# Kernel tuning notes

Hardware: AMD Instinct MI355X
Metric: run time of the kernel (lower is better)

The kernel has to match this reference:

```python
import jax, jax.numpy as jnp
import numpy as np

IN, OUT, RANK = 512, 1024, 8
STEPS = 8  # fixed-step RK4 integration of the geodesic ODE over t in [0, 1]


def setup_inputs() -> dict:
    key = jax.random.key(0)
    ks = jax.random.split(key, 8)
    scale = 0.05
    x = jax.random.normal(ks[0], (8, 4096, IN), jnp.float32)
    # orthogonal init of U_0 [OUT, IN] (orthonormal columns, tall matrix)
    U0 = jnp.linalg.qr(jax.random.normal(ks[1], (OUT, IN), jnp.float32))[0]
    Wa = scale * jax.random.normal(ks[2], (IN, RANK), jnp.float32)
    La = scale * jax.random.normal(ks[3], (IN, RANK), jnp.float32)
    Ra = scale * jax.random.normal(ks[4], (IN, RANK), jnp.float32)
    Wb = scale * jax.random.normal(ks[5], (IN, RANK), jnp.float32)
    Lb = scale * jax.random.normal(ks[6], (OUT - IN, RANK), jnp.float32)
    Rb = scale * jax.random.normal(ks[7], (IN, RANK), jnp.float32)
    return {"x": x, "U0": U0, "Wa": Wa, "La": La, "Ra": Ra,
            "Wb": Wb, "Lb": Lb, "Rb": Rb}


def _geodesic_solve(U0, A, G):
    # Integrate dU/dt = U @ A + G, U(0) = U0, with RK4 over unit time.
    dt = 1.0 / STEPS
    f = lambda U: U @ A + G
    def step(U, _):
        k1 = f(U)
        k2 = f(U + 0.5 * dt * k1)
        k3 = f(U + 0.5 * dt * k2)
        k4 = f(U + dt * k3)
        return U + (dt / 6.0) * (k1 + 2.0 * k2 + 2.0 * k3 + k4), None
    U, _ = jax.lax.scan(step, U0, None, length=STEPS)
    return U


def reference(x, U0, Wa, La, Ra, Wb, Lb, Rb):
    # z: pooled context [B, IN]
    z = x.mean(axis=1)
    # low-rank controller -> skew-symmetric Lie-algebra drift A [IN, IN]
    a = z @ Wa                                      # [B, R]
    A = jnp.einsum('br,ir,jr->bij', a, La, Ra)      # [B, IN, IN]
    A_avg = (A - jnp.swapaxes(A, 1, 2)).mean(axis=0)  # skew, batch-averaged
    # low-rank forcing B [B, OUT-IN, IN], batch-averaged
    b = z @ Wb                                      # [B, R]
    B_avg = jnp.einsum('br,or,jr->boj', b, Lb, Rb).mean(axis=0)
    # pad top with zeros -> G [OUT, IN]
    G = jnp.concatenate([jnp.zeros((IN, IN), x.dtype), B_avg], axis=0)
    # geodesic/Lie ODE solve for the dynamic weight W [OUT, IN]
    W = _geodesic_solve(U0, A_avg, G)
    # final dense projection
    return x @ W.T
```

## Files before the change

### kernel.cpp

```cpp
#include <hip/hip_runtime.h>
#include <hip/hip_bf16.h>
#include <type_traits>
#include <cstdint>

#define IN_DIM   512
#define OUT_DIM  1024
#define MROWS    32768

typedef float f32x4 __attribute__((ext_vector_type(4)));
typedef short s8vec __attribute__((ext_vector_type(8)));
typedef __bf16 b8vec __attribute__((ext_vector_type(8)));

template <typename V, typename = void>
struct mfma_ok : std::false_type {};
template <typename V>
struct mfma_ok<V, std::void_t<decltype(__builtin_amdgcn_mfma_f32_16x16x32_bf16(
    std::declval<V>(), std::declval<V>(), std::declval<f32x4>(), 0, 0, 0))>>
    : std::true_type {};
using frag_t = std::conditional_t<mfma_ok<s8vec>::value, s8vec, b8vec>;

__device__ __forceinline__ void async_copy16(void* lds, const void* g) {
    __builtin_amdgcn_global_load_lds(
        (const __attribute__((address_space(1))) void*)(uintptr_t)g,
        (__attribute__((address_space(3))) void*)(uint32_t)(uintptr_t)lds,
        16, 0, 0);
}

__device__ __forceinline__ unsigned short f2bf(float f) {
    unsigned int u = __float_as_uint(f);
    unsigned int r = (u + 0x7fffu + ((u >> 16) & 1u)) >> 16;
    return (unsigned short)r;
}

__global__ void __launch_bounds__(256) geo_k1(const float* __restrict__ x,
                                              unsigned short* __restrict__ xh,
                                              const float* __restrict__ Wa,
                                              const float* __restrict__ Wb,
                                              float* __restrict__ part) {
    const int tid  = threadIdx.x;
    const int c4   = (tid & 127) * 4;
    const int half = tid >> 7;
    const int r0   = blockIdx.x * 32 + half * 16;
    float4 s = {0.f, 0.f, 0.f, 0.f};
    for (int i = 0; i < 16; ++i) {
        const size_t base = (size_t)(r0 + i) * IN_DIM + c4;
        float4 v = *(const float4*)(x + base);
        s.x += v.x; s.y += v.y; s.z += v.z; s.w += v.w;
        ushort4 h;
        h.x = f2bf(v.x); h.y = f2bf(v.y); h.z = f2bf(v.z); h.w = f2bf(v.w);
        *(ushort4*)(xh + base) = h;
    }
    const float* wa = Wa + (size_t)c4 * 8;
    const float* wb = Wb + (size_t)c4 * 8;
    float av[8], bv[8];
#pragma unroll
    for (int r = 0; r < 8; ++r) {
        av[r] = s.x * wa[r] + s.y * wa[8 + r] + s.z * wa[16 + r] + s.w * wa[24 + r];
        bv[r] = s.x * wb[r] + s.y * wb[8 + r] + s.z * wb[16 + r] + s.w * wb[24 + r];
    }
#pragma unroll
    for (int off = 32; off; off >>= 1) {
#pragma unroll
        for (int r = 0; r < 8; ++r) {
            av[r] += __shfl_xor(av[r], off, 64);
            bv[r] += __shfl_xor(bv[r], off, 64);
        }
    }
    __shared__ float wred[4][16];
    const int lane = tid & 63, wave = tid >> 6;
    if (lane == 0) {
#pragma unroll
        for (int r = 0; r < 8; ++r) { wred[wave][r] = av[r]; wred[wave][8 + r] = bv[r]; }
    }
    __syncthreads();
    if (tid < 16)
        part[(size_t)blockIdx.x * 16 + tid] =
            wred[0][tid] + wred[1][tid] + wred[2][tid] + wred[3][tid];
}

__device__ __forceinline__ void mm16(float (*D)[16], float (*A)[16], float (*B)[16]) {
    const int tid = threadIdx.x;
    const int i = tid >> 4, j = tid & 15;
    float s = 0.f;
#pragma unroll
    for (int k = 0; k < 16; ++k) s += A[i][k] * B[k][j];
    __syncthreads();
    D[i][j] = s;
    __syncthreads();
}

__global__ void __launch_bounds__(256) geo_k2(const float* __restrict__ part,
                                              const float* __restrict__ La,
                                              const float* __restrict__ Ra,
                                              const float* __restrict__ Lb,
                                              const float* __restrict__ Rb,
                                              float* __restrict__ Vws,
                                              float* __restrict__ Lbp,
                                              float* __restrict__ VPws,
                                              float* __restrict__ RRws) {
    __shared__ float sV[IN_DIM][16];
    __shared__ float sRb[IN_DIM][8];
    __shared__ float red2[16][16];
    __shared__ float gs[16];
    __shared__ float G16[16][16], Jm[16][16];
    __shared__ float C2m[16][16], C3m[16][16], C4m[16][16];
    __shared__ float Cp[16][16], Cq[16][16];
    __shared__ float Pi[16][16], Xi[16][16], T1[16][16], T2[16][16], Ct[16][16];
    __shared__ float Zm[8][16], Em[8][16];
    const int tid = threadIdx.x;
    const int i = tid >> 4, j = tid & 15;

    {
        const int u = tid & 15, c = tid >> 4;
        float s = 0.f;
        for (int q = 0; q < 64; ++q) s += part[(size_t)(c * 64 + q) * 16 + u];
        red2[c][u] = s;
    }
    __syncthreads();
    if (tid < 16) {
        float s = 0.f;
#pragma unroll
        for (int c = 0; c < 16; ++c) s += red2[c][tid];
        gs[tid] = s * (1.0f / 32768.0f);
    }
    __syncthreads();

    for (int rr = 0; rr < 2; ++rr) {
        const int row = tid * 2 + rr;
#pragma unroll
        for (int r = 0; r < 8; ++r) {
            const float vl = gs[r] * La[row * 8 + r];
            const float vr = Ra[row * 8 + r];
            sV[row][r]     = vl;
            sV[row][8 + r] = vr;
            Vws[row * 16 + r]     = vl;
            Vws[row * 16 + 8 + r] = vr;
            sRb[row][r] = Rb[row * 8 + r];
            Lbp[row * 8 + r] = gs[8 + r] * Lb[row * 8 + r];
        }
    }
    __syncthreads();

    {
        float s = 0.f;
        for (int k = 0; k < IN_DIM; ++k) s += sV[k][i] * sV[k][j];
        G16[i][j] = s;
        float jm = 0.f;
        if (i < 8 && j == i + 8) jm = 1.f;
        if (i >= 8 && j == i - 8) jm = -1.f;
        Jm[i][j] = jm;
    }
    if (tid < 128) {
        const int r = tid >> 4, u = tid & 15;
        float s = 0.f;
        for (int k = 0; k < IN_DIM; ++k) s += sRb[k][r] * sV[k][u];
        Zm[r][u] = s;
    }
    __syncthreads();

    mm16(T1, Jm, G16);  mm16(C2m, T1, Jm);
    mm16(T1, C2m, G16); mm16(C3m, T1, Jm);
    mm16(T1, C3m, G16); mm16(C4m, T1, Jm);

    const float h  = 0.125f;
    const float c1 = h, c2 = h * h * 0.5f, c3 = h * h * h * (1.f / 6.f),
                c4 = h * h * h * h * (1.f / 24.f);
    Cp[i][j] = c1 * Jm[i][j] + c2 * C2m[i][j] + c3 * C3m[i][j] + c4 * C4m[i][j];
    Cq[i][j] = c2 * Jm[i][j] + c3 * C2m[i][j] + c4 * C3m[i][j];
    Xi[i][j] = 0.f;
    __syncthreads();
    Pi[i][j] = Cp[i][j];
    __syncthreads();

    for (int it = 0; it < 7; ++it) {
        mm16(T1, Pi, G16);
        mm16(T2, T1, Cp);
        const float pij = Pi[i][j];
        Xi[i][j] += pij;
        Pi[i][j] = pij + Cp[i][j] + T2[i][j];
        __syncthreads();
    }

    mm16(T1, Cq, G16);
    mm16(T2, T1, Xi);
    Ct[i][j] = 8.f * Cq[i][j] + h * Xi[i][j] + T2[i][j];
    __syncthreads();

    if (tid < 128) {
        const int r = tid >> 4, u = tid & 15;
        float s = 0.f;
#pragma unroll
        for (int t = 0; t < 16; ++t) s += Zm[r][t] * Ct[t][u];
        Em[r][u] = s;
    }
    __syncthreads();

#pragma unroll
    for (int rr = 0; rr < 2; ++rr) {
        const int row = tid * 2 + rr;
        float v[16];
#pragma unroll
        for (int k = 0; k < 16; ++k) v[k] = sV[row][k];
#pragma unroll
        for (int u = 0; u < 16; ++u) {
            float s = 0.f;
#pragma unroll
            for (int k = 0; k < 16; ++k) s += v[k] * Pi[k][u];
            VPws[row * 16 + u] = s;
        }
#pragma unroll
        for (int r = 0; r < 8; ++r) {
            float s = sRb[row][r];
#pragma unroll
            for (int u = 0; u < 16; ++u) s += Em[r][u] * v[u];
            RRws[r * IN_DIM + row] = s;
        }
    }
}

__global__ void __launch_bounds__(256) geo_k34(const float* __restrict__ U0,
                                               const float* __restrict__ Vws,
                                               const float* __restrict__ VPws,
                                               const float* __restrict__ Lbp,
                                               const float* __restrict__ RRws,
                                               unsigned short* __restrict__ wh) {
    const int o   = blockIdx.x;
    const int tid = threadIdx.x;
    const int j0  = tid * 2;
    const float2 u0 = *(const float2*)(U0 + (size_t)o * IN_DIM + j0);

    const float* vpa = VPws + j0 * 16;
    const float* vpb = vpa + 16;
    float p[16];
#pragma unroll
    for (int u = 0; u < 16; ++u) p[u] = u0.x * vpa[u] + u0.y * vpb[u];
#pragma unroll
    for (int off = 32; off; off >>= 1) {
#pragma unroll
        for (int u = 0; u < 16; ++u) p[u] += __shfl_xor(p[u], off, 64);
    }
    __shared__ float wred[4][16];
    __shared__ float sY[16];
    const int lane = tid & 63, wave = tid >> 6;
    if (lane == 0) {
#pragma unroll
        for (int u = 0; u < 16; ++u) wred[wave][u] = p[u];
    }
    __syncthreads();
    if (tid < 16) sY[tid] = wred[0][tid] + wred[1][tid] + wred[2][tid] + wred[3][tid];
    __syncthreads();

    const float* va = Vws + j0 * 16;
    const float* vb = va + 16;
    float w0 = u0.x, w1 = u0.y;
#pragma unroll
    for (int u = 0; u < 16; ++u) {
        const float s = sY[u];
        w0 += s * va[u];
        w1 += s * vb[u];
    }
    if (o >= IN_DIM) {
        const int op = o - IN_DIM;
#pragma unroll
        for (int r = 0; r < 8; ++r) {
            const float lb = Lbp[op * 8 + r];
            w0 += lb * RRws[r * IN_DIM + j0];
            w1 += lb * RRws[r * IN_DIM + j0 + 1];
        }
    }
    ushort2 hv;
    hv.x = f2bf(w0); hv.y = f2bf(w1);
    *(ushort2*)(wh + (size_t)o * IN_DIM + j0) = hv;
}

__global__ void __launch_bounds__(256) geo_k5_gemm(const __hip_bfloat16* __restrict__ A,
                                                   const __hip_bfloat16* __restrict__ B,
                                                   float* __restrict__ C) {
    __shared__ __hip_bfloat16 As[128 * 64];
    __shared__ __hip_bfloat16 Bs[128 * 64];
    const int tid  = threadIdx.x;
    const int m0   = blockIdx.x * 128;
    const int n0   = blockIdx.y * 128;
    const int lane = tid & 63;
    const int wave = tid >> 6;
    const int wm   = (wave >> 1) * 64;
    const int wn   = (wave & 1) * 64;

    const int rowoff = lane >> 3;
    const int gcol   = ((lane & 7) ^ rowoff) * 8;
    const __hip_bfloat16* gA[4];
    const __hip_bfloat16* gB[4];
    char* lA[4];
    char* lB[4];
#pragma unroll
    for (int j2 = 0; j2 < 4; ++j2) {
        const int ri  = wave * 4 + j2;
        const int row = ri * 8 + rowoff;
        gA[j2] = A + (size_t)(m0 + row) * IN_DIM + gcol;
        gB[j2] = B + (size_t)(n0 + row) * IN_DIM + gcol;
        lA[j2] = (char*)As + ri * 1024 + lane * 16;
        lB[j2] = (char*)Bs + ri * 1024 + lane * 16;
    }

    f32x4 acc[4][4];
#pragma unroll
    for (int t = 0; t < 4; ++t)
#pragma unroll
        for (int s = 0; s < 4; ++s) acc[t][s] = (f32x4){0.f, 0.f, 0.f, 0.f};

    const int frow = lane & 15;
    const int fsw  = lane & 7;
    const int fk   = lane >> 4;

    for (int kt = 0; kt < 8; ++kt) {
        const int k0 = kt * 64;
        __syncthreads();
#pragma unroll
        for (int j2 = 0; j2 < 4; ++j2) {
            async_copy16(lA[j2], gA[j2] + k0);
            async_copy16(lB[j2], gB[j2] + k0);
        }
        __syncthreads();

#pragma unroll
        for (int h = 0; h < 2; ++h) {
            frag_t af[4], bfr[4];
#pragma unroll
            for (int t = 0; t < 4; ++t)
                af[t] = *(const frag_t*)((const char*)As +
                        (size_t)(wm + t * 16 + frow) * 128 + (((h * 4 + fk) ^ fsw) * 16));
#pragma unroll
            for (int s = 0; s < 4; ++s)
                bfr[s] = *(const frag_t*)((const char*)Bs +
                        (size_t)(wn + s * 16 + frow) * 128 + (((h * 4 + fk) ^ fsw) * 16));
#pragma unroll
            for (int t = 0; t < 4; ++t)
#pragma unroll
                for (int s = 0; s < 4; ++s)
                    acc[t][s] = __builtin_amdgcn_mfma_f32_16x16x32_bf16(af[t], bfr[s], acc[t][s], 0, 0, 0);
        }
    }

    const int cm = m0 + wm + (lane >> 4) * 4;
    const int cn = n0 + wn + (lane & 15);
#pragma unroll
    for (int t = 0; t < 4; ++t)
#pragma unroll
        for (int s = 0; s < 4; ++s)
#pragma unroll
            for (int v = 0; v < 4; ++v)
                C[(size_t)(cm + t * 16 + v) * OUT_DIM + cn + s * 16] = acc[t][s][v];
}

extern "C" void kernel_launch(void* const* d_in, const int* in_sizes, int n_in,
                              void* d_out, int out_size, void* d_ws, size_t ws_size,
                              hipStream_t stream) {
    const float* x  = (const float*)d_in[0];
    const float* U0 = (const float*)d_in[1];
    const float* Wa = (const float*)d_in[2];
    const float* La = (const float*)d_in[3];
    const float* Ra = (const float*)d_in[4];
    const float* Wb = (const float*)d_in[5];
    const float* Lb = (const float*)d_in[6];
    const float* Rb = (const float*)d_in[7];
    float* out = (float*)d_out;

    char* ws = (char*)d_ws;
    unsigned short* xh  = (unsigned short*)(ws);
    unsigned short* wh  = (unsigned short*)(ws + 33554432);
    float* part = (float*)(ws + 34603008);
    float* Vws  = (float*)(ws + 34668544);
    float* Lbp  = (float*)(ws + 34701312);
    float* RRws = (float*)(ws + 34717696);
    float* VPws = (float*)(ws + 34734080);

    geo_k1<<<1024, 256, 0, stream>>>(x, xh, Wa, Wb, part);
    geo_k2<<<1, 256, 0, stream>>>(part, La, Ra, Lb, Rb, Vws, Lbp, VPws, RRws);
    geo_k34<<<1024, 256, 0, stream>>>(U0, Vws, VPws, Lbp, RRws, wh);
    geo_k5_gemm<<<dim3(256, 8), 256, 0, stream>>>((const __hip_bfloat16*)xh,
                                                  (const __hip_bfloat16*)wh, out);
}
```

Measured before the change: 280.6 us.

## Rewrite final GEMM with 256x256 tiles and 4-stage async LDS pipeline

The final x@W^T GEMM now uses 512-thread blocks computing 256x256 tiles with 32-wide K steps, kept in a 4-deep ring of LDS buffers loaded asynchronously. Explicit vmcnt waits replace the load-then-sync pattern so global loads overlap MFMA work. The launch is also remapped so that blocks sharing an XCD work on neighbouring M tiles, and MFMA sections get raised wave priority. The cost is 128KB of LDS per block and 128 accumulator registers per thread, which limits occupancy, and the hand-counted waitcnt/barrier sequencing has to be exactly right.

Measured after the change: 272.7 us. 2.8% less time.

```diff
diff --git a/kernel.cpp b/kernel.cpp
--- a/kernel.cpp
+++ b/kernel.cpp
@@ -273,83 +273,117 @@
     *(ushort2*)(wh + (size_t)o * IN_DIM + j0) = hv;
 }
 
-__global__ void __launch_bounds__(256) geo_k5_gemm(const __hip_bfloat16* __restrict__ A,
-                                                   const __hip_bfloat16* __restrict__ B,
-                                                   float* __restrict__ C) {
-    __shared__ __hip_bfloat16 As[128 * 64];
-    __shared__ __hip_bfloat16 Bs[128 * 64];
-    const int tid  = threadIdx.x;
-    const int m0   = blockIdx.x * 128;
-    const int n0   = blockIdx.y * 128;
-    const int lane = tid & 63;
-    const int wave = tid >> 6;
-    const int wm   = (wave >> 1) * 64;
-    const int wn   = (wave & 1) * 64;
-
-    const int rowoff = lane >> 3;
-    const int gcol   = ((lane & 7) ^ rowoff) * 8;
-    const __hip_bfloat16* gA[4];
-    const __hip_bfloat16* gB[4];
-    char* lA[4];
-    char* lB[4];
-#pragma unroll
-    for (int j2 = 0; j2 < 4; ++j2) {
-        const int ri  = wave * 4 + j2;
-        const int row = ri * 8 + rowoff;
-        gA[j2] = A + (size_t)(m0 + row) * IN_DIM + gcol;
-        gB[j2] = B + (size_t)(n0 + row) * IN_DIM + gcol;
-        lA[j2] = (char*)As + ri * 1024 + lane * 16;
-        lB[j2] = (char*)Bs + ri * 1024 + lane * 16;
-    }
-
-    f32x4 acc[4][4];
-#pragma unroll
-    for (int t = 0; t < 4; ++t)
-#pragma unroll
-        for (int s = 0; s < 4; ++s) acc[t][s] = (f32x4){0.f, 0.f, 0.f, 0.f};
-
-    const int frow = lane & 15;
-    const int fsw  = lane & 7;
-    const int fk   = lane >> 4;
-
-    for (int kt = 0; kt < 8; ++kt) {
-        const int k0 = kt * 64;
-        __syncthreads();
-#pragma unroll
-        for (int j2 = 0; j2 < 4; ++j2) {
-            async_copy16(lA[j2], gA[j2] + k0);
-            async_copy16(lB[j2], gB[j2] + k0);
-        }
-        __syncthreads();
-
-#pragma unroll
-        for (int h = 0; h < 2; ++h) {
-            frag_t af[4], bfr[4];
-#pragma unroll
-            for (int t = 0; t < 4; ++t)
-                af[t] = *(const frag_t*)((const char*)As +
-                        (size_t)(wm + t * 16 + frow) * 128 + (((h * 4 + fk) ^ fsw) * 16));
-#pragma unroll
-            for (int s = 0; s < 4; ++s)
-                bfr[s] = *(const frag_t*)((const char*)Bs +
-                        (size_t)(wn + s * 16 + frow) * 128 + (((h * 4 + fk) ^ fsw) * 16));
-#pragma unroll
-            for (int t = 0; t < 4; ++t)
-#pragma unroll
-                for (int s = 0; s < 4; ++s)
-                    acc[t][s] = __builtin_amdgcn_mfma_f32_16x16x32_bf16(af[t], bfr[s], acc[t][s], 0, 0, 0);
-        }
-    }
-
-    const int cm = m0 + wm + (lane >> 4) * 4;
-    const int cn = n0 + wn + (lane & 15);
-#pragma unroll
-    for (int t = 0; t < 4; ++t)
+__device__ __forceinline__ void k5_frag_loads(const char* lds, int sb, int aoff, int boff,
+                                              frag_t (&a)[8], frag_t (&b)[4]) {
+#pragma unroll
+    for (int u = 0; u < 8; ++u)
+        a[u] = *(const frag_t*)(lds + sb + aoff + u * 1024);
+#pragma unroll
+    for (int s = 0; s < 4; ++s)
+        b[s] = *(const frag_t*)(lds + sb + boff + s * 1024);
+}
+
+template <int VM, bool DO_STAGE>
+__device__ __forceinline__ void k5_step(char* lds, int t,
+                                        const __hip_bfloat16* gA0, const __hip_bfloat16* gA1,
+                                        const __hip_bfloat16* gB0, const __hip_bfloat16* gB1,
+                                        int ldsA0, int ldsA1, int aoff, int boff,
+                                        f32x4 (&acc)[8][4]) {
+    if constexpr (VM == 12)     asm volatile("s_waitcnt vmcnt(12)" ::: "memory");
+    else if constexpr (VM == 8) asm volatile("s_waitcnt vmcnt(8)"  ::: "memory");
+    else if constexpr (VM == 4) asm volatile("s_waitcnt vmcnt(4)"  ::: "memory");
+    else                        asm volatile("s_waitcnt vmcnt(0)"  ::: "memory");
+    __builtin_amdgcn_s_barrier();
+    __builtin_amdgcn_sched_barrier(0);
+
+    const int sb = (t & 3) * 32768;
+    frag_t a[8], b[4];
+    k5_frag_loads(lds, sb, aoff, boff, a, b);
+
+    __builtin_amdgcn_s_setprio(1);
+#pragma unroll
+    for (int u = 0; u < 8; ++u)
 #pragma unroll
         for (int s = 0; s < 4; ++s)
+            acc[u][s] = __builtin_amdgcn_mfma_f32_16x16x32_bf16(a[u], b[s], acc[u][s], 0, 0, 0);
+    __builtin_amdgcn_s_setprio(0);
+
+    asm volatile("s_waitcnt lgkmcnt(0)" ::: "memory");
+    __builtin_amdgcn_sched_barrier(0);
+    __builtin_amdgcn_s_barrier();
+
+    if constexpr (DO_STAGE) {
+        const int ko = (t + 4) * 32;
+        async_copy16(lds + sb + ldsA0,         gA0 + ko);
+        async_copy16(lds + sb + ldsA1,         gA1 + ko);
+        async_copy16(lds + sb + 16384 + ldsA0, gB0 + ko);
+        async_copy16(lds + sb + 16384 + ldsA1, gB1 + ko);
+    }
+}
+
+__global__ void __launch_bounds__(512, 2) geo_k5_gemm(const __hip_bfloat16* __restrict__ A,
+                                                      const __hip_bfloat16* __restrict__ B,
+                                                      float* __restrict__ C) {
+    __shared__ alignas(16) char lds[131072];
+    const int tid = threadIdx.x;
+    const int l = tid & 63, w = tid >> 6;
+
+    const int bid = blockIdx.x;
+    const int xcd = bid & 7;
+    const int loc = bid >> 3;
+    const int m0  = (xcd * 16 + (loc >> 2)) * 256;
+    const int n0  = (loc & 3) * 256;
+
+    const int swz   = (((l & 3) ^ ((l >> 3) & 3)) * 8);
+    const int rloc0 = w * 32 + (l >> 2);
+    const int rloc1 = rloc0 + 16;
+    const __hip_bfloat16* gA0 = A + (size_t)(m0 + rloc0) * IN_DIM + swz;
+    const __hip_bfloat16* gA1 = A + (size_t)(m0 + rloc1) * IN_DIM + swz;
+    const __hip_bfloat16* gB0 = B + (size_t)(n0 + rloc0) * IN_DIM + swz;
+    const __hip_bfloat16* gB1 = B + (size_t)(n0 + rloc1) * IN_DIM + swz;
+    const int ldsA0 = w * 2048 + l * 16;
+    const int ldsA1 = ldsA0 + 1024;
+
+    const int lane15 = l & 15;
+    const int s_r    = (lane15 >> 1) & 3;
+    const int rdch   = ((l >> 4) ^ s_r) * 16;
+    const int wmoff  = (w >> 2) * 128;
+    const int wnoff  = (w & 3) * 64;
+    const int aoff   = (wmoff + lane15) * 64 + rdch;
+    const int boff   = 16384 + (wnoff + lane15) * 64 + rdch;
+
+    f32x4 acc[8][4];
+#pragma unroll
+    for (int u = 0; u < 8; ++u)
+#pragma unroll
+        for (int s = 0; s < 4; ++s) acc[u][s] = (f32x4){0.f, 0.f, 0.f, 0.f};
+
+#pragma unroll
+    for (int p = 0; p < 4; ++p) {
+        const int sb = p * 32768;
+        const int ko = p * 32;
+        async_copy16(lds + sb + ldsA0,         gA0 + ko);
+        async_copy16(lds + sb + ldsA1,         gA1 + ko);
+        async_copy16(lds + sb + 16384 + ldsA0, gB0 + ko);
+        async_copy16(lds + sb + 16384 + ldsA1, gB1 + ko);
+    }
+
+    for (int t = 0; t < 12; ++t)
+        k5_step<12, true>(lds, t, gA0, gA1, gB0, gB1, ldsA0, ldsA1, aoff, boff, acc);
+    k5_step<12, false>(lds, 12, gA0, gA1, gB0, gB1, ldsA0, ldsA1, aoff, boff, acc);
+    k5_step<8,  false>(lds, 13, gA0, gA1, gB0, gB1, ldsA0, ldsA1, aoff, boff, acc);
+    k5_step<4,  false>(lds, 14, gA0, gA1, gB0, gB1, ldsA0, ldsA1, aoff, boff, acc);
+    k5_step<0,  false>(lds, 15, gA0, gA1, gB0, gB1, ldsA0, ldsA1, aoff, boff, acc);
+
+    const int cm = m0 + wmoff + (l >> 4) * 4;
+    const int cn = n0 + wnoff + lane15;
+#pragma unroll
+    for (int u = 0; u < 8; ++u)
+#pragma unroll
+        for (int s = 0; s < 4; ++s)
 #pragma unroll
             for (int v = 0; v < 4; ++v)
-                C[(size_t)(cm + t * 16 + v) * OUT_DIM + cn + s * 16] = acc[t][s][v];
+                C[(size_t)(cm + u * 16 + v) * OUT_DIM + cn + s * 16] = acc[u][s][v];
 }
 
 extern "C" void kernel_launch(void* const* d_in, const int* in_sizes, int n_in,
@@ -377,6 +411,6 @@
     geo_k1<<<1024, 256, 0, stream>>>(x, xh, Wa, Wb, part);
     geo_k2<<<1, 256, 0, stream>>>(part, La, Ra, Lb, Rb, Vws, Lbp, VPws, RRws);
     geo_k34<<<1024, 256, 0, stream>>>(U0, Vws, VPws, Lbp, RRws, wh);
-    geo_k5_gemm<<<dim3(256, 8), 256, 0, stream>>>((const __hip_bfloat16*)xh,
-                                                  (const __hip_bfloat16*)wh, out);
-}
+    geo_k5_gemm<<<512, 512, 0, stream>>>((const __hip_bfloat16*)xh,
+                                         (const __hip_bfloat16*)wh, out);
+}
```
